# Kernel tuning notes

Hardware: AMD Instinct MI355X
Metric: run time of the kernel (lower is better)

Reference implementation:

```python
import jax, jax.numpy as jnp
import numpy as np

H = 16
D = 64  # head_dim = 1024 // 16
SCALE = D ** -0.5


def setup_inputs() -> dict:
    key = jax.random.key(0)
    ks = jax.random.split(key, 12)
    B, N, C = 2, 2048, 1024
    s = C ** -0.5
    return {
        "hidden_states": jax.random.normal(ks[0], (B, N, C), jnp.float32),
        "pos_embeds": jax.random.normal(ks[1], (B, N, C), jnp.float32),
        "Wq": jax.random.normal(ks[2], (C, C), jnp.float32) * s,
        "bq": jnp.zeros((C,), jnp.float32),
        "Wk": jax.random.normal(ks[3], (C, C), jnp.float32) * s,
        "bk": jnp.zeros((C,), jnp.float32),
        "Wv": jax.random.normal(ks[4], (C, C), jnp.float32) * s,
        "bv": jnp.zeros((C,), jnp.float32),
        "Wpos": jax.random.normal(ks[5], (C, C), jnp.float32) * s,
        "pos_bias_u": jax.random.normal(ks[6], (H, D), jnp.float32) * 0.1,
        "pos_bias_v": jax.random.normal(ks[7], (H, D), jnp.float32) * 0.1,
        "Wo": jax.random.normal(ks[8], (C, C), jnp.float32) * s,
        "bo": jnp.zeros((C,), jnp.float32),
    }


def reference(hidden_states, pos_embeds, Wq, bq, Wk, bk, Wv, bv, Wpos,
              pos_bias_u, pos_bias_v, Wo, bo):
    B, N, C = hidden_states.shape
    # projections (torch Linear: y = x @ W.T + b), split heads -> (B, N, H, D)
    q = (hidden_states @ Wq.T + bq).reshape(B, N, H, D)
    k = (hidden_states @ Wk.T + bk).reshape(B, N, H, D)
    v = (hidden_states @ Wv.T + bv).reshape(B, N, H, D)
    p = (pos_embeds @ Wpos.T).reshape(B, N, H, D)
    # relative-position biased logits: matrix_ac + matrix_bd
    q_u = q + pos_bias_u  # (B,N,H,D) + (H,D)
    q_v = q + pos_bias_v
    ac = jnp.einsum('bnhd,bmhd->bhnm', q_u, k)
    bd = jnp.einsum('bnhd,bmhd->bhnm', q_v, p)
    attn = jax.nn.softmax((ac + bd) * SCALE, axis=-1)  # (B,H,N,N)
    out = jnp.einsum('bhnm,bmhd->bnhd', attn, v).reshape(B, N, C)
    return out @ Wo.T + bo
```

## Files before the change

### kernel.cpp

```cpp
#include <hip/hip_runtime.h>
#include <hip/hip_bf16.h>


typedef short bf16x8 __attribute__((ext_vector_type(8)));
typedef float f32x4 __attribute__((ext_vector_type(4)));

#define BB 2
#define NN 2048
#define CC 1024
#define HH 16
#define DD 64
#define MM (BB * NN)
#define SC2E 0.18033688f

__device__ __forceinline__ unsigned short f2bf(float f) {
    union { float f; unsigned int u; } x; x.f = f;
    unsigned int r = x.u + 0x7FFFu + ((x.u >> 16) & 1u);
    return (unsigned short)(r >> 16);
}

__device__ __forceinline__ float bf2f(unsigned short s) {
    union { unsigned int u; float f; } x; x.u = ((unsigned int)s) << 16;
    return x.f;
}

__device__ __forceinline__ unsigned int pk2(float a, float b) {
    __hip_bfloat162 h = __float22bfloat162_rn(make_float2(a, b));
    unsigned int u; __builtin_memcpy(&u, &h, 4); return u;
}

typedef __attribute__((address_space(1))) const unsigned int* gas1_t;
typedef __attribute__((address_space(3))) unsigned int* las3_t;

__device__ __forceinline__ void gload_lds16(const unsigned short* g, unsigned short* l) {
    __builtin_amdgcn_global_load_lds((gas1_t)g, (las3_t)l, 16, 0, 0);
}

struct CastArgs {
    const float* src[7];
    unsigned short* dst[7];
    int n4[7];
};
__global__ __launch_bounds__(256) void cast_all(CastArgs a) {
    const int seg = blockIdx.y;
    const int i = blockIdx.x * 256 + threadIdx.x;
    if (i >= a.n4[seg]) return;
    float4 v = ((const float4*)a.src[seg])[i];
    uint2 u;
    u.x = pk2(v.x, v.y);
    u.y = pk2(v.z, v.w);
    ((uint2*)a.dst[seg])[i] = u;
}

struct GemmBatch {
    const unsigned short* A[4];
    const unsigned short* B[4];
    unsigned short* out[4];
    const float* bias[4];
};
__global__ __launch_bounds__(256) void gemm_qkvp(GemmBatch g) {
    constexpr int K = CC;
    __shared__ unsigned short Sh[2 * 128 * 32];
    unsigned short* As = Sh;
    unsigned short* Bs = Sh + 128 * 32;
    const int z = blockIdx.z;
    const unsigned short* __restrict__ A = g.A[z];
    const unsigned short* __restrict__ B = g.B[z];
    unsigned short* __restrict__ out = g.out[z];
    const float* __restrict__ bias = g.bias[z];

    const int t = threadIdx.x;
    const int w = t >> 6, lane = t & 63, l15 = lane & 15, quad = lane >> 4;
    const int m0 = blockIdx.x * 128, n0 = blockIdx.y * 128;
    const int wm = (w >> 1) * 64, wn = (w & 1) * 64;

    f32x4 acc[4][4];
#pragma unroll
    for (int i = 0; i < 4; ++i)
#pragma unroll
        for (int j = 0; j < 4; ++j)
#pragma unroll
            for (int r = 0; r < 4; ++r) acc[i][j][r] = 0.f;

    for (int kb = 0; kb < K; kb += 32) {
        __syncthreads();
#pragma unroll
        for (int j = 0; j < 2; ++j) {
            int id = j * 256 + t;
            int row = id >> 2, c4 = (id & 3) * 8;
            gload_lds16(&A[(size_t)(m0 + row) * K + kb + c4], &As[id * 8]);
            gload_lds16(&B[(size_t)(n0 + row) * K + kb + c4], &Bs[id * 8]);
        }
        __syncthreads();
        bf16x8 af[4], bfr[4];
#pragma unroll
        for (int i = 0; i < 4; ++i)
            af[i] = *(const bf16x8*)&As[(wm + i * 16 + l15) * 32 + quad * 8];
#pragma unroll
        for (int j = 0; j < 4; ++j)
            bfr[j] = *(const bf16x8*)&Bs[(wn + j * 16 + l15) * 32 + quad * 8];
#pragma unroll
        for (int i = 0; i < 4; ++i)
#pragma unroll
            for (int j = 0; j < 4; ++j)
                acc[i][j] = __builtin_amdgcn_mfma_f32_16x16x32_bf16(af[i], bfr[j], acc[i][j], 0, 0, 0);
    }

    if (z != 2) {
        const float sc = (z == 0) ? SC2E : 1.f;
#pragma unroll
        for (int i = 0; i < 4; ++i)
#pragma unroll
            for (int j = 0; j < 4; ++j) {
                const int col = n0 + wn + j * 16 + l15;
                const int row_base = m0 + wm + i * 16 + quad * 4;
                const float bc = bias ? bias[col] : 0.f;
#pragma unroll
                for (int r = 0; r < 4; ++r)
                    out[(size_t)(row_base + r) * CC + col] = f2bf((acc[i][j][r] + bc) * sc);
            }
    } else {
        __syncthreads();
        unsigned short* Tr = &Sh[w * 1152];
        const int bI = (m0 + wm) >> 11, nseq0 = (m0 + wm) & 2047;
        const int colL = lane >> 3;
        const int mL = (lane & 7) * 8;
#pragma unroll
        for (int j = 0; j < 4; ++j) {
            const int col = n0 + wn + j * 16 + l15;
            const float bc = bias[col];
#pragma unroll
            for (int i = 0; i < 4; ++i) {
                uint2 pk;
                pk.x = pk2(acc[i][j][0] + bc, acc[i][j][1] + bc);
                pk.y = pk2(acc[i][j][2] + bc, acc[i][j][3] + bc);
                *(uint2*)&Tr[l15 * 72 + i * 16 + quad * 4] = pk;
            }
#pragma unroll
            for (int p = 0; p < 2; ++p) {
                const int cl = p * 8 + colL;
                uint4 vv = *(const uint4*)&Tr[cl * 72 + mL];
                const int gcol = n0 + wn + j * 16 + cl;
                const int hh = gcol >> 6, dd = gcol & 63;
                *(uint4*)&out[((size_t)(bI * 16 + hh) * 64 + dd) * 2048 + nseq0 + mL] = vv;
            }
        }
    }
}

__global__ __launch_bounds__(256) void fuse_kpc(const unsigned short* __restrict__ k,
                                                const unsigned short* __restrict__ pp,
                                                const float* __restrict__ pbu,
                                                const float* __restrict__ pbv,
                                                unsigned short* __restrict__ kp,
                                                float* __restrict__ c) {
    const int gw = (blockIdx.x * 256 + threadIdx.x) >> 6;
    const int lane = threadIdx.x & 63;
    const int row = gw >> 4, h = gw & 15;
    const size_t off = (size_t)row * CC + h * 64 + lane;
    const float kv = bf2f(k[off]), pv = bf2f(pp[off]);
    kp[off] = f2bf(kv + pv);
    float val = pbu[h * 64 + lane] * kv + pbv[h * 64 + lane] * pv;
#pragma unroll
    for (int o = 1; o < 64; o <<= 1) val += __shfl_xor(val, o);
    if (lane == 0) {
        const int b = row >> 11, n = row & 2047;
        c[((size_t)(b * HH + h)) * NN + n] = val * SC2E;
    }
}

__global__ __launch_bounds__(512) void attn_kernel(const unsigned short* __restrict__ q,
                                                   const unsigned short* __restrict__ kp,
                                                   const unsigned short* __restrict__ vt,
                                                   const float* __restrict__ cb,
                                                   unsigned short* __restrict__ att) {
    __shared__ unsigned short Ks[2][128 * 64];
    __shared__ unsigned short Vs[2][64 * 128];
    __shared__ unsigned short Ps[8][16 * 64];

    const int t = threadIdx.x;
    const int w = t >> 6, lane = t & 63, l15 = lane & 15, quad = lane >> 4;
    const int qt = blockIdx.x, h = blockIdx.y, b = blockIdx.z;
    const int e3 = l15 & 7;

    bf16x8 qf[2];
    {
        const int qrow = qt * 128 + w * 16 + l15;
        const size_t qoff = ((size_t)(b * NN + qrow) * HH + h) * DD;
#pragma unroll
        for (int c2 = 0; c2 < 2; ++c2)
            qf[c2] = *(const bf16x8*)&q[qoff + c2 * 32 + quad * 8];
    }

    f32x4 oT[4];
    float l_lane = 0.f;
#pragma unroll
    for (int db = 0; db < 4; ++db)
#pragma unroll
        for (int r = 0; r < 4; ++r) oT[db][r] = 0.f;

    const size_t kbase = (size_t)b * NN * CC + (size_t)h * DD;
    const size_t vbase = (size_t)(b * HH + h) * DD * NN;
    const size_t cbase = (size_t)(b * HH + h) * NN;

    int krow[2], kgc[2], vd[2], vgc[2];
#pragma unroll
    for (int j = 0; j < 2; ++j) {
        const int id = j * 512 + t;
        krow[j] = id >> 3;
        kgc[j] = ((id & 7) ^ (krow[j] & 7)) * 8;
        vd[j] = id >> 4;
        vgc[j] = ((id & 15) ^ (vd[j] & 7)) * 8;
    }

#pragma unroll
    for (int j = 0; j < 2; ++j) {
        const int id = j * 512 + t;
        gload_lds16(&kp[kbase + (size_t)krow[j] * CC + kgc[j]], &Ks[0][id * 8]);
        gload_lds16(&vt[vbase + (size_t)vd[j] * NN + vgc[j]], &Vs[0][id * 8]);
    }

    for (int kt = 0; kt < NN / 128; ++kt) {
        const int cur = kt & 1;
        __syncthreads();
        if (kt + 1 < NN / 128) {
#pragma unroll
            for (int j = 0; j < 2; ++j) {
                const int id = j * 512 + t;
                gload_lds16(&kp[kbase + (size_t)((kt + 1) * 128 + krow[j]) * CC + kgc[j]],
                            &Ks[cur ^ 1][id * 8]);
                gload_lds16(&vt[vbase + (size_t)vd[j] * NN + (kt + 1) * 128 + vgc[j]],
                            &Vs[cur ^ 1][id * 8]);
            }
        }

        f32x4 c8r[8];
#pragma unroll
        for (int t8 = 0; t8 < 8; ++t8)
            c8r[t8] = *(const f32x4*)&cb[cbase + kt * 128 + t8 * 16 + quad * 4];

#pragma unroll
        for (int half = 0; half < 2; ++half) {
            f32x4 s[4];
#pragma unroll
            for (int t4 = 0; t4 < 4; ++t4) s[t4] = c8r[half * 4 + t4];

            __builtin_amdgcn_s_setprio(1);
#pragma unroll
            for (int t4 = 0; t4 < 4; ++t4) {
                const int row = half * 64 + t4 * 16 + l15;
#pragma unroll
                for (int c2 = 0; c2 < 2; ++c2) {
                    bf16x8 kf = *(const bf16x8*)&Ks[cur][row * 64 + (((c2 * 4 + quad) ^ e3) * 8)];
                    s[t4] = __builtin_amdgcn_mfma_f32_16x16x32_bf16(kf, qf[c2], s[t4], 0, 0, 0);
                }
            }
            __builtin_amdgcn_s_setprio(0);

            float rs = 0.f;
#pragma unroll
            for (int t4 = 0; t4 < 4; ++t4)
#pragma unroll
                for (int r = 0; r < 4; ++r) {
                    float pv = exp2f(s[t4][r]);
                    s[t4][r] = pv;
                    rs += pv;
                }
            l_lane += rs;
#pragma unroll
            for (int t4 = 0; t4 < 4; ++t4) {
                uint2 pk;
                pk.x = pk2(s[t4][0], s[t4][1]);
                pk.y = pk2(s[t4][2], s[t4][3]);
                const int blk = t4 * 2 + (quad >> 1);
                *(uint2*)&Ps[w][l15 * 64 + ((blk ^ e3) * 8) + (quad & 1) * 4] = pk;
            }

            __builtin_amdgcn_s_setprio(1);
#pragma unroll
            for (int c2 = 0; c2 < 2; ++c2) {
                bf16x8 pf = *(const bf16x8*)&Ps[w][l15 * 64 + (((c2 * 4 + quad) ^ e3) * 8)];
#pragma unroll
                for (int db = 0; db < 4; ++db) {
                    bf16x8 vf = *(const bf16x8*)&Vs[cur][(db * 16 + l15) * 128 +
                                                         (((half * 8 + c2 * 4 + quad) ^ e3) * 8)];
                    oT[db] = __builtin_amdgcn_mfma_f32_16x16x32_bf16(vf, pf, oT[db], 0, 0, 0);
                }
            }
            __builtin_amdgcn_s_setprio(0);
        }
    }

    float l = l_lane;
    l += __shfl_xor(l, 16);
    l += __shfl_xor(l, 32);
    const float inv = 1.f / l;
    const int qrow = qt * 128 + w * 16 + l15;
    const size_t ob = ((size_t)(b * NN + qrow) * HH + h) * DD;
#pragma unroll
    for (int db = 0; db < 4; ++db) {
        uint2 pk;
        pk.x = pk2(oT[db][0] * inv, oT[db][1] * inv);
        pk.y = pk2(oT[db][2] * inv, oT[db][3] * inv);
        *(uint2*)&att[ob + db * 16 + quad * 4] = pk;
    }
}

__global__ __launch_bounds__(256) void gemm_out(const unsigned short* __restrict__ A,
                                                const unsigned short* __restrict__ B,
                                                float* __restrict__ out,
                                                const float* __restrict__ bias) {
    constexpr int K = CC;
    __shared__ unsigned short As[128 * 32];
    __shared__ unsigned short Bs[64 * 32];
    const int t = threadIdx.x;
    const int w = t >> 6, lane = t & 63, l15 = lane & 15, quad = lane >> 4;
    const int m0 = blockIdx.x * 128, n0 = blockIdx.y * 64;
    const int wm = (w >> 1) * 64, wn = (w & 1) * 32;

    f32x4 acc[4][2];
#pragma unroll
    for (int i = 0; i < 4; ++i)
#pragma unroll
        for (int j = 0; j < 2; ++j)
#pragma unroll
            for (int r = 0; r < 4; ++r) acc[i][j][r] = 0.f;

    for (int kb = 0; kb < K; kb += 32) {
        __syncthreads();
#pragma unroll
        for (int j = 0; j < 2; ++j) {
            int id = j * 256 + t;
            int row = id >> 2, c4 = (id & 3) * 8;
            gload_lds16(&A[(size_t)(m0 + row) * K + kb + c4], &As[id * 8]);
        }
        {
            int row = t >> 2, c4 = (t & 3) * 8;
            gload_lds16(&B[(size_t)(n0 + row) * K + kb + c4], &Bs[t * 8]);
        }
        __syncthreads();
        bf16x8 af[4], bfr[2];
#pragma unroll
        for (int i = 0; i < 4; ++i)
            af[i] = *(const bf16x8*)&As[(wm + i * 16 + l15) * 32 + quad * 8];
#pragma unroll
        for (int j = 0; j < 2; ++j)
            bfr[j] = *(const bf16x8*)&Bs[(wn + j * 16 + l15) * 32 + quad * 8];
#pragma unroll
        for (int i = 0; i < 4; ++i)
#pragma unroll
            for (int j = 0; j < 2; ++j)
                acc[i][j] = __builtin_amdgcn_mfma_f32_16x16x32_bf16(af[i], bfr[j], acc[i][j], 0, 0, 0);
    }

#pragma unroll
    for (int i = 0; i < 4; ++i)
#pragma unroll
        for (int j = 0; j < 2; ++j) {
            const int col = n0 + wn + j * 16 + l15;
            const int row_base = m0 + wm + i * 16 + quad * 4;
            const float bc = bias[col];
#pragma unroll
            for (int r = 0; r < 4; ++r)
                out[(size_t)(row_base + r) * CC + col] = acc[i][j][r] + bc;
        }
}

extern "C" void kernel_launch(void* const* d_in, const int* in_sizes, int n_in,
                              void* d_out, int out_size, void* d_ws, size_t ws_size,
                              hipStream_t stream) {
    const float* hs   = (const float*)d_in[0];
    const float* pos  = (const float*)d_in[1];
    const float* Wq   = (const float*)d_in[2];
    const float* bq   = (const float*)d_in[3];
    const float* Wk   = (const float*)d_in[4];
    const float* bk   = (const float*)d_in[5];
    const float* Wv   = (const float*)d_in[6];
    const float* bv   = (const float*)d_in[7];
    const float* Wpos = (const float*)d_in[8];
    const float* pbu  = (const float*)d_in[9];
    const float* pbv  = (const float*)d_in[10];
    const float* Wo   = (const float*)d_in[11];
    const float* bo   = (const float*)d_in[12];
    float* out = (float*)d_out;

    const size_t nHS = (size_t)MM * CC;
    const size_t nW  = (size_t)CC * CC;

    unsigned short* p = (unsigned short*)d_ws;
    unsigned short* hsb  = p;            p += nHS;
    unsigned short* posb = p;            p += nHS;
    unsigned short* wqb  = p;            p += nW;
    unsigned short* wkb  = p;            p += nW;
    unsigned short* wvb  = p;            p += nW;
    unsigned short* wpb  = p;            p += nW;
    unsigned short* wob  = p;            p += nW;
    unsigned short* qsb  = p;            p += nHS;
    unsigned short* kbf  = p;            p += nHS;
    unsigned short* pbf  = p;            p += nHS;
    unsigned short* kpb  = p;            p += nHS;
    unsigned short* vtb  = p;            p += nHS;
    float* cb = (float*)p;               p += (size_t)BB * HH * NN * 2;
    unsigned short* attb = hsb;

    CastArgs ca;
    ca.src[0] = hs;   ca.dst[0] = hsb;  ca.n4[0] = (int)(nHS / 4);
    ca.src[1] = pos;  ca.dst[1] = posb; ca.n4[1] = (int)(nHS / 4);
    ca.src[2] = Wq;   ca.dst[2] = wqb;  ca.n4[2] = (int)(nW / 4);
    ca.src[3] = Wk;   ca.dst[3] = wkb;  ca.n4[3] = (int)(nW / 4);
    ca.src[4] = Wv;   ca.dst[4] = wvb;  ca.n4[4] = (int)(nW / 4);
    ca.src[5] = Wpos; ca.dst[5] = wpb;  ca.n4[5] = (int)(nW / 4);
    ca.src[6] = Wo;   ca.dst[6] = wob;  ca.n4[6] = (int)(nW / 4);
    dim3 cgrid((unsigned)(nHS / 4 / 256), 7);
    cast_all<<<cgrid, 256, 0, stream>>>(ca);

    GemmBatch gb;
    gb.A[0] = hsb;  gb.B[0] = wqb; gb.out[0] = qsb; gb.bias[0] = bq;
    gb.A[1] = hsb;  gb.B[1] = wkb; gb.out[1] = kbf; gb.bias[1] = bk;
    gb.A[2] = hsb;  gb.B[2] = wvb; gb.out[2] = vtb; gb.bias[2] = bv;
    gb.A[3] = posb; gb.B[3] = wpb; gb.out[3] = pbf; gb.bias[3] = nullptr;
    dim3 ggrid(MM / 128, CC / 128, 4);
    gemm_qkvp<<<ggrid, 256, 0, stream>>>(gb);

    fuse_kpc<<<MM * HH / 4, 256, 0, stream>>>(kbf, pbf, pbu, pbv, kpb, cb);

    dim3 agrid(NN / 128, HH, BB);
    attn_kernel<<<agrid, 512, 0, stream>>>(qsb, kpb, vtb, cb, attb);

    dim3 ogrid(MM / 128, CC / 64);
    gemm_out<<<ogrid, 256, 0, stream>>>(attb, wob, out, bo);
}
```

Before: 257.7 us.

## Process two 16-row query blocks per wave to double K/V tile reuse

Each wave in the attention kernel now computes 32 query rows instead of 16, so each block covers 256 rows and the grid halves. Every K and V fragment loaded from shared memory feeds two MFMAs, which halves global and LDS traffic per unit of work. In exchange, register and LDS use rise and the block count drops to one per CU, which can reduce latency hiding.

```diff
diff --git a/kernel.cpp b/kernel.cpp
--- a/kernel.cpp
+++ b/kernel.cpp
@@ -176,28 +176,31 @@
                                                    unsigned short* __restrict__ att) {
     __shared__ unsigned short Ks[2][128 * 64];
     __shared__ unsigned short Vs[2][64 * 128];
-    __shared__ unsigned short Ps[8][16 * 64];
+    __shared__ unsigned short Ps[8][32 * 64];
 
     const int t = threadIdx.x;
     const int w = t >> 6, lane = t & 63, l15 = lane & 15, quad = lane >> 4;
     const int qt = blockIdx.x, h = blockIdx.y, b = blockIdx.z;
     const int e3 = l15 & 7;
 
-    bf16x8 qf[2];
-    {
-        const int qrow = qt * 128 + w * 16 + l15;
+    bf16x8 qf[2][2];
+#pragma unroll
+    for (int qb = 0; qb < 2; ++qb) {
+        const int qrow = qt * 256 + w * 32 + qb * 16 + l15;
         const size_t qoff = ((size_t)(b * NN + qrow) * HH + h) * DD;
 #pragma unroll
         for (int c2 = 0; c2 < 2; ++c2)
-            qf[c2] = *(const bf16x8*)&q[qoff + c2 * 32 + quad * 8];
-    }
-
-    f32x4 oT[4];
-    float l_lane = 0.f;
+            qf[qb][c2] = *(const bf16x8*)&q[qoff + c2 * 32 + quad * 8];
+    }
+
+    f32x4 oT[4][2];
+    float l_lane[2] = {0.f, 0.f};
 #pragma unroll
     for (int db = 0; db < 4; ++db)
 #pragma unroll
-        for (int r = 0; r < 4; ++r) oT[db][r] = 0.f;
+        for (int qb = 0; qb < 2; ++qb)
+#pragma unroll
+            for (int r = 0; r < 4; ++r) oT[db][qb][r] = 0.f;
 
     const size_t kbase = (size_t)b * NN * CC + (size_t)h * DD;
     const size_t vbase = (size_t)(b * HH + h) * DD * NN;
@@ -241,9 +244,12 @@
 
 #pragma unroll
         for (int half = 0; half < 2; ++half) {
-            f32x4 s[4];
-#pragma unroll
-            for (int t4 = 0; t4 < 4; ++t4) s[t4] = c8r[half * 4 + t4];
+            f32x4 s[2][4];
+#pragma unroll
+            for (int t4 = 0; t4 < 4; ++t4) {
+                s[0][t4] = c8r[half * 4 + t4];
+                s[1][t4] = c8r[half * 4 + t4];
+            }
 
             __builtin_amdgcn_s_setprio(1);
 #pragma unroll
@@ -252,57 +258,70 @@
 #pragma unroll
                 for (int c2 = 0; c2 < 2; ++c2) {
                     bf16x8 kf = *(const bf16x8*)&Ks[cur][row * 64 + (((c2 * 4 + quad) ^ e3) * 8)];
-                    s[t4] = __builtin_amdgcn_mfma_f32_16x16x32_bf16(kf, qf[c2], s[t4], 0, 0, 0);
+#pragma unroll
+                    for (int qb = 0; qb < 2; ++qb)
+                        s[qb][t4] = __builtin_amdgcn_mfma_f32_16x16x32_bf16(kf, qf[qb][c2], s[qb][t4], 0, 0, 0);
                 }
             }
             __builtin_amdgcn_s_setprio(0);
 
-            float rs = 0.f;
-#pragma unroll
-            for (int t4 = 0; t4 < 4; ++t4)
-#pragma unroll
-                for (int r = 0; r < 4; ++r) {
-                    float pv = exp2f(s[t4][r]);
-                    s[t4][r] = pv;
-                    rs += pv;
+#pragma unroll
+            for (int qb = 0; qb < 2; ++qb) {
+                float rs = 0.f;
+#pragma unroll
+                for (int t4 = 0; t4 < 4; ++t4)
+#pragma unroll
+                    for (int r = 0; r < 4; ++r) {
+                        float pv = exp2f(s[qb][t4][r]);
+                        s[qb][t4][r] = pv;
+                        rs += pv;
+                    }
+                l_lane[qb] += rs;
+#pragma unroll
+                for (int t4 = 0; t4 < 4; ++t4) {
+                    uint2 pk;
+                    pk.x = pk2(s[qb][t4][0], s[qb][t4][1]);
+                    pk.y = pk2(s[qb][t4][2], s[qb][t4][3]);
+                    const int blk = t4 * 2 + (quad >> 1);
+                    *(uint2*)&Ps[w][(qb * 16 + l15) * 64 + ((blk ^ e3) * 8) + (quad & 1) * 4] = pk;
                 }
-            l_lane += rs;
-#pragma unroll
-            for (int t4 = 0; t4 < 4; ++t4) {
-                uint2 pk;
-                pk.x = pk2(s[t4][0], s[t4][1]);
-                pk.y = pk2(s[t4][2], s[t4][3]);
-                const int blk = t4 * 2 + (quad >> 1);
-                *(uint2*)&Ps[w][l15 * 64 + ((blk ^ e3) * 8) + (quad & 1) * 4] = pk;
             }
 
             __builtin_amdgcn_s_setprio(1);
 #pragma unroll
             for (int c2 = 0; c2 < 2; ++c2) {
-                bf16x8 pf = *(const bf16x8*)&Ps[w][l15 * 64 + (((c2 * 4 + quad) ^ e3) * 8)];
+                bf16x8 pf[2];
+#pragma unroll
+                for (int qb = 0; qb < 2; ++qb)
+                    pf[qb] = *(const bf16x8*)&Ps[w][(qb * 16 + l15) * 64 + (((c2 * 4 + quad) ^ e3) * 8)];
 #pragma unroll
                 for (int db = 0; db < 4; ++db) {
                     bf16x8 vf = *(const bf16x8*)&Vs[cur][(db * 16 + l15) * 128 +
                                                          (((half * 8 + c2 * 4 + quad) ^ e3) * 8)];
-                    oT[db] = __builtin_amdgcn_mfma_f32_16x16x32_bf16(vf, pf, oT[db], 0, 0, 0);
+#pragma unroll
+                    for (int qb = 0; qb < 2; ++qb)
+                        oT[db][qb] = __builtin_amdgcn_mfma_f32_16x16x32_bf16(vf, pf[qb], oT[db][qb], 0, 0, 0);
                 }
             }
             __builtin_amdgcn_s_setprio(0);
         }
     }
 
-    float l = l_lane;
-    l += __shfl_xor(l, 16);
-    l += __shfl_xor(l, 32);
-    const float inv = 1.f / l;
-    const int qrow = qt * 128 + w * 16 + l15;
-    const size_t ob = ((size_t)(b * NN + qrow) * HH + h) * DD;
-#pragma unroll
-    for (int db = 0; db < 4; ++db) {
-        uint2 pk;
-        pk.x = pk2(oT[db][0] * inv, oT[db][1] * inv);
-        pk.y = pk2(oT[db][2] * inv, oT[db][3] * inv);
-        *(uint2*)&att[ob + db * 16 + quad * 4] = pk;
+#pragma unroll
+    for (int qb = 0; qb < 2; ++qb) {
+        float l = l_lane[qb];
+        l += __shfl_xor(l, 16);
+        l += __shfl_xor(l, 32);
+        const float inv = 1.f / l;
+        const int qrow = qt * 256 + w * 32 + qb * 16 + l15;
+        const size_t ob = ((size_t)(b * NN + qrow) * HH + h) * DD;
+#pragma unroll
+        for (int db = 0; db < 4; ++db) {
+            uint2 pk;
+            pk.x = pk2(oT[db][qb][0] * inv, oT[db][qb][1] * inv);
+            pk.y = pk2(oT[db][qb][2] * inv, oT[db][qb][3] * inv);
+            *(uint2*)&att[ob + db * 16 + quad * 4] = pk;
+        }
     }
 }
 
@@ -424,7 +443,7 @@
 
     fuse_kpc<<<MM * HH / 4, 256, 0, stream>>>(kbf, pbf, pbu, pbv, kpb, cb);
 
-    dim3 agrid(NN / 128, HH, BB);
+    dim3 agrid(NN / 256, HH, BB);
     attn_kernel<<<agrid, 512, 0, stream>>>(qsb, kpb, vtb, cb, attb);
 
     dim3 ogrid(MM / 128, CC / 64);
```

Measured after the change: 263.8 us. 1.02x slower.

## Double-buffer LDS staging and swizzle tile order in projection GEMMs

Applied to the files above, without the earlier changes.

Both the QKVP projection GEMM and the output GEMM now use two LDS buffers, so the next K-slice is loaded while MFMAs run on the current one. Each loop iteration drops from two barriers to one. Block-to-tile mapping is also remapped in groups of 8 to improve L2 reuse of operand rows. The single barrier relies on async global-to-LDS loads finishing before the next barrier, which risks a race if the load helper does not wait at the barrier. LDS use per block also doubles.

```diff
diff --git a/kernel.cpp b/kernel.cpp
--- a/kernel.cpp
+++ b/kernel.cpp
@@ -60,9 +60,7 @@
 };
 __global__ __launch_bounds__(256) void gemm_qkvp(GemmBatch g) {
     constexpr int K = CC;
-    __shared__ unsigned short Sh[2 * 128 * 32];
-    unsigned short* As = Sh;
-    unsigned short* Bs = Sh + 128 * 32;
+    __shared__ unsigned short Sh[4 * 128 * 32];
     const int z = blockIdx.z;
     const unsigned short* __restrict__ A = g.A[z];
     const unsigned short* __restrict__ B = g.B[z];
@@ -71,7 +69,9 @@
 
     const int t = threadIdx.x;
     const int w = t >> 6, lane = t & 63, l15 = lane & 15, quad = lane >> 4;
-    const int m0 = blockIdx.x * 128, n0 = blockIdx.y * 128;
+    const int id = blockIdx.y * 32 + blockIdx.x;
+    const int tile = (id & 7) * 32 + (id >> 3);
+    const int m0 = (tile & 31) * 128, n0 = (tile >> 5) * 128;
     const int wm = (w >> 1) * 64, wn = (w & 1) * 64;
 
     f32x4 acc[4][4];
@@ -82,16 +82,25 @@
 #pragma unroll
             for (int r = 0; r < 4; ++r) acc[i][j][r] = 0.f;
 
-    for (int kb = 0; kb < K; kb += 32) {
+    auto STAGE = [&](int b, int kb) {
+        unsigned short* As = &Sh[b * 8192];
+        unsigned short* Bs = &Sh[b * 8192 + 4096];
+#pragma unroll
+        for (int j = 0; j < 2; ++j) {
+            int idt = j * 256 + t;
+            int row = idt >> 2, c4 = (idt & 3) * 8;
+            gload_lds16(&A[(size_t)(m0 + row) * K + kb + c4], &As[idt * 8]);
+            gload_lds16(&B[(size_t)(n0 + row) * K + kb + c4], &Bs[idt * 8]);
+        }
+    };
+
+    STAGE(0, 0);
+    for (int ki = 0; ki < K / 32; ++ki) {
+        const int cur = ki & 1;
         __syncthreads();
-#pragma unroll
-        for (int j = 0; j < 2; ++j) {
-            int id = j * 256 + t;
-            int row = id >> 2, c4 = (id & 3) * 8;
-            gload_lds16(&A[(size_t)(m0 + row) * K + kb + c4], &As[id * 8]);
-            gload_lds16(&B[(size_t)(n0 + row) * K + kb + c4], &Bs[id * 8]);
-        }
-        __syncthreads();
+        if (ki + 1 < K / 32) STAGE(cur ^ 1, (ki + 1) * 32);
+        const unsigned short* As = &Sh[cur * 8192];
+        const unsigned short* Bs = &Sh[cur * 8192 + 4096];
         bf16x8 af[4], bfr[4];
 #pragma unroll
         for (int i = 0; i < 4; ++i)
@@ -311,11 +320,13 @@
                                                 float* __restrict__ out,
                                                 const float* __restrict__ bias) {
     constexpr int K = CC;
-    __shared__ unsigned short As[128 * 32];
-    __shared__ unsigned short Bs[64 * 32];
+    __shared__ unsigned short As[2][128 * 32];
+    __shared__ unsigned short Bs[2][64 * 32];
     const int t = threadIdx.x;
     const int w = t >> 6, lane = t & 63, l15 = lane & 15, quad = lane >> 4;
-    const int m0 = blockIdx.x * 128, n0 = blockIdx.y * 64;
+    const int id = blockIdx.y * 32 + blockIdx.x;
+    const int tile = (id & 7) * 64 + (id >> 3);
+    const int m0 = (tile & 31) * 128, n0 = (tile >> 5) * 64;
     const int wm = (w >> 1) * 64, wn = (w & 1) * 32;
 
     f32x4 acc[4][2];
@@ -326,26 +337,31 @@
 #pragma unroll
             for (int r = 0; r < 4; ++r) acc[i][j][r] = 0.f;
 
-    for (int kb = 0; kb < K; kb += 32) {
-        __syncthreads();
+    auto STAGE = [&](int bf, int kb) {
 #pragma unroll
         for (int j = 0; j < 2; ++j) {
-            int id = j * 256 + t;
-            int row = id >> 2, c4 = (id & 3) * 8;
-            gload_lds16(&A[(size_t)(m0 + row) * K + kb + c4], &As[id * 8]);
+            int idt = j * 256 + t;
+            int row = idt >> 2, c4 = (idt & 3) * 8;
+            gload_lds16(&A[(size_t)(m0 + row) * K + kb + c4], &As[bf][idt * 8]);
         }
         {
             int row = t >> 2, c4 = (t & 3) * 8;
-            gload_lds16(&B[(size_t)(n0 + row) * K + kb + c4], &Bs[t * 8]);
-        }
+            gload_lds16(&B[(size_t)(n0 + row) * K + kb + c4], &Bs[bf][t * 8]);
+        }
+    };
+
+    STAGE(0, 0);
+    for (int ki = 0; ki < K / 32; ++ki) {
+        const int cur = ki & 1;
         __syncthreads();
+        if (ki + 1 < K / 32) STAGE(cur ^ 1, (ki + 1) * 32);
         bf16x8 af[4], bfr[2];
 #pragma unroll
         for (int i = 0; i < 4; ++i)
-            af[i] = *(const bf16x8*)&As[(wm + i * 16 + l15) * 32 + quad * 8];
+            af[i] = *(const bf16x8*)&As[cur][(wm + i * 16 + l15) * 32 + quad * 8];
 #pragma unroll
         for (int j = 0; j < 2; ++j)
-            bfr[j] = *(const bf16x8*)&Bs[(wn + j * 16 + l15) * 32 + quad * 8];
+            bfr[j] = *(const bf16x8*)&Bs[cur][(wn + j * 16 + l15) * 32 + quad * 8];
 #pragma unroll
         for (int i = 0; i < 4; ++i)
 #pragma unroll
```

Measured after the change: 275.2 us. +6.8%, slower.
